# Performance work log

Measured on AMD Instinct MI355X. Metric: run time of the kernel, lower is better.

The kernel has to match this reference:

```python
import jax, jax.numpy as jnp
import numpy as np

NEG_SLOPE = 0.2  # PyG GATConv default negative_slope
EPS = 1e-16


def gat_conv(x, edge_index, W, att_src, att_dst, bias, heads, out_c, concat):
    """Faithful PyG GATConv forward (add_self_loops=True).
    x: [N, F_in], edge_index: [2, E] (row 0 = src, row 1 = dst),
    W: [heads*out_c, F_in], att_src/att_dst: [1, heads, out_c], bias: [out]
    """
    N = x.shape[0]
    loop = jnp.arange(N, dtype=edge_index.dtype)
    src = jnp.concatenate([edge_index[0], loop])
    dst = jnp.concatenate([edge_index[1], loop])

    h = (x @ W.T).reshape(N, heads, out_c)            # [N, H, C]
    a_src = jnp.sum(h * att_src, axis=-1)             # [N, H]
    a_dst = jnp.sum(h * att_dst, axis=-1)             # [N, H]

    e = jax.nn.leaky_relu(a_src[src] + a_dst[dst], NEG_SLOPE)   # [E+N, H]
    # numerically-stable segment softmax over incoming edges of dst
    m = jax.ops.segment_max(e, dst, num_segments=N)             # [N, H]
    p = jnp.exp(e - m[dst])
    denom = jax.ops.segment_sum(p, dst, num_segments=N)         # [N, H]
    alpha = p / (denom[dst] + EPS)                              # [E+N, H]

    out = jax.ops.segment_sum(h[src] * alpha[:, :, None], dst, num_segments=N)  # [N, H, C]
    out = out.reshape(N, heads * out_c) if concat else out.mean(axis=1)
    return out + bias


def setup_inputs() -> dict:
    key = jax.random.key(0)
    ks = jax.random.split(key, 11)
    N, E = 100_000, 1_600_000
    in_dim, hid, heads = 128, 64, 2
    s = 0.1
    x = jax.random.normal(ks[0], (N, in_dim), jnp.float32)
    edge_index_l2 = jax.random.randint(ks[1], (2, E), 0, N, dtype=jnp.int32)
    edge_index_l1 = jax.random.randint(ks[2], (2, E), 0, N, dtype=jnp.int32)
    # layer gat_l2: in_dim -> hid per head, heads=2, concat=True
    W2 = jax.random.normal(ks[3], (heads * hid, in_dim), jnp.float32) * s
    att_src2 = jax.random.normal(ks[4], (1, heads, hid), jnp.float32) * s
    att_dst2 = jax.random.normal(ks[5], (1, heads, hid), jnp.float32) * s
    b2 = jnp.zeros((heads * hid,), jnp.float32)
    # layer gat_l1: hid*heads -> hid, 1 head, concat=False
    W1 = jax.random.normal(ks[6], (hid, heads * hid), jnp.float32) * s
    att_src1 = jax.random.normal(ks[7], (1, 1, hid), jnp.float32) * s
    att_dst1 = jax.random.normal(ks[8], (1, 1, hid), jnp.float32) * s
    b1 = jnp.zeros((hid,), jnp.float32)
    return {
        "x": x,
        "edge_index_l1": edge_index_l1,
        "edge_index_l2": edge_index_l2,
        "W2": W2, "att_src2": att_src2, "att_dst2": att_dst2, "b2": b2,
        "W1": W1, "att_src1": att_src1, "att_dst1": att_dst1, "b1": b1,
    }


def reference(x, edge_index_l1, edge_index_l2, W2, att_src2, att_dst2, b2,
              W1, att_src1, att_dst1, b1):
    h = jax.nn.elu(gat_conv(x, edge_index_l2, W2, att_src2, att_dst2, b2,
                            heads=2, out_c=64, concat=True))    # [N, 128]
    h = jax.nn.elu(gat_conv(h, edge_index_l1, W1, att_src1, att_dst1, b1,
                            heads=1, out_c=64, concat=False))   # [N, 64]
    return h
```

## Files before the change

### kernel.cpp

```cpp
#include <hip/hip_runtime.h>
#include <hip/hip_bf16.h>
#include <math.h>

#define LRELU_SLOPE 0.2f
#define EPS 1e-16f
#define BUCK_SHIFT 8
#define BUCK_NODES 256
#define MAXBUCK 512

typedef __hip_bfloat16 bf16;
typedef __attribute__((ext_vector_type(8))) short bf16x8;
typedef __attribute__((ext_vector_type(4))) float f32x4;

__device__ inline float lrelu(float v) { return v > 0.f ? v : LRELU_SLOPE * v; }
__device__ inline float bflo(unsigned u) { return __uint_as_float(u << 16); }
__device__ inline float bfhi(unsigned u) { return __uint_as_float(u & 0xffff0000u); }
__device__ inline short f2bf(float f) {
  bf16 t = __float2bfloat16(f);
  return *reinterpret_cast<short*>(&t);
}
__device__ inline unsigned pack2(float lo, float hi) {
  return ((unsigned)(unsigned short)f2bf(hi) << 16) | (unsigned)(unsigned short)f2bf(lo);
}

__global__ void prep_kernel(const float* __restrict__ W2, unsigned short* __restrict__ Wb2,
                            const float* __restrict__ W1, unsigned short* __restrict__ Wb1,
                            int* __restrict__ gcur, int ngc) {
  int idx = blockIdx.x * blockDim.x + threadIdx.x;
  if (idx < ngc) gcur[idx] = 0;
  if (idx < 16384) {
    Wb2[idx] = (unsigned short)f2bf(W2[idx]);
  } else {
    int i = idx - 16384;
    if (i < 8192) Wb1[i] = (unsigned short)f2bf(W1[i]);
  }
}

template <int EPB>
__global__ __launch_bounds__(256) void partition_both_kernel(
    const int* __restrict__ ei2, int E2, int* __restrict__ gcur2, int* __restrict__ slab2,
    const int* __restrict__ ei1, int E1, int* __restrict__ gcur1, int* __restrict__ slab1,
    int cap, int nbuck, int nblk2) {
  __shared__ int cnt[MAXBUCK];
  __shared__ int sbase[MAXBUCK];
  const int tid = threadIdx.x;
  const bool l2 = (int)blockIdx.x < nblk2;
  const int bid = l2 ? blockIdx.x : blockIdx.x - nblk2;
  const int* ei = l2 ? ei2 : ei1;
  const int E = l2 ? E2 : E1;
  int* gcur = l2 ? gcur2 : gcur1;
  int* part = l2 ? slab2 : slab1;
  for (int t = tid; t < nbuck; t += 256) cnt[t] = 0;
  __syncthreads();
  const int e0 = bid * EPB;
  constexpr int KPT = EPB / 256;
  int sv[KPT], dv[KPT];
#pragma unroll
  for (int k = 0; k < KPT; k++) {
    int e = e0 + tid + k * 256;
    if (e < E) {
      sv[k] = ei[e];
      dv[k] = ei[E + e];
      atomicAdd(&cnt[dv[k] >> BUCK_SHIFT], 1);
    } else {
      dv[k] = -1;
    }
  }
  __syncthreads();
  for (int t = tid; t < nbuck; t += 256) {
    int c = cnt[t];
    if (c) sbase[t] = atomicAdd(&gcur[t], c);
    cnt[t] = 0;
  }
  __syncthreads();
#pragma unroll
  for (int k = 0; k < KPT; k++) {
    if (dv[k] >= 0) {
      int b = dv[k] >> BUCK_SHIFT;
      int pos = sbase[b] + atomicAdd(&cnt[b], 1);
      if (pos < cap) part[(size_t)b * cap + pos] = (sv[k] << 8) | (dv[k] & (BUCK_NODES - 1));
    }
  }
}

template <int H>
__global__ __launch_bounds__(256) void csr_build_kernel(
    int* __restrict__ slab, const int* __restrict__ gcur, int cap,
    const float* __restrict__ asrc, const float* __restrict__ adst, float* __restrict__ pcsr,
    int plane, int* __restrict__ rowbeg, int* __restrict__ rowend, int N) {
  extern __shared__ char smem[];
  int* s_sd = (int*)smem;
  int* hist = (int*)(s_sd + cap);
  int* histp = hist + 256;
  int* escanp = histp + 256;
  int* cur = escanp + 256;
  int* wtot = cur + 256;
  float* s_ad = (float*)(wtot + 4);

  const int b = blockIdx.x;
  const int tid = threadIdx.x;
  const int lane = tid & 63;
  const int wid = tid >> 6;
  const int nb0 = b << BUCK_SHIFT;
  const int nn = min(BUCK_NODES, N - nb0);
  const int cnt = min(gcur[b], cap - 7 * BUCK_NODES);
  const int B = b * cap;
  int* eidx = slab;

  hist[tid] = 0;
  cur[tid] = 0;
  for (int t = tid; t < nn * H; t += 256) s_ad[t] = adst[(size_t)nb0 * H + t];
  __syncthreads();
  for (int i = tid; i < cnt; i += 256) {
    int pr = slab[(size_t)B + i];
    s_sd[i] = pr;
    atomicAdd(&hist[pr & (BUCK_NODES - 1)], 1);
  }
  __syncthreads();
  const int h0 = hist[tid];
  const int hp = (h0 + 7) & ~7;
  histp[tid] = hp;
  int inc = hp;
#pragma unroll
  for (int off = 1; off < 64; off <<= 1) {
    int t = __shfl_up(inc, off);
    if (lane >= off) inc += t;
  }
  if (lane == 63) wtot[wid] = inc;
  __syncthreads();
  int base = 0;
  for (int w = 0; w < wid; w++) base += wtot[w];
  escanp[tid] = inc + base;
  if (tid < nn) {
    rowbeg[nb0 + tid] = B + inc + base - hp;
    rowend[nb0 + tid] = B + inc + base;
  }
  __syncthreads();
  for (int i = tid; i < cnt; i += 256) {
    int pr = s_sd[i];
    int d8 = pr & (BUCK_NODES - 1);
    int s = pr >> 8;
    int slot = B + (escanp[d8] - histp[d8]) + atomicAdd(&cur[d8], 1);
    eidx[slot] = s;
    if constexpr (H == 2) {
      float2 a = *(const float2*)&asrc[2 * (size_t)s];
      float2 ad = *(const float2*)&s_ad[2 * d8];
      pcsr[slot] = __expf(lrelu(a.x + ad.x));
      pcsr[plane + slot] = __expf(lrelu(a.y + ad.y));
    } else {
      pcsr[slot] = __expf(lrelu(asrc[s] + s_ad[d8]));
    }
  }
  if (tid < nn) {
    int pb = B + escanp[tid] - histp[tid];
    for (int k = h0; k < hp; k++) {
      eidx[pb + k] = nb0 + tid;
      pcsr[pb + k] = 0.f;
      if constexpr (H == 2) pcsr[plane + pb + k] = 0.f;
    }
  }
}

template <int M, int H, bool SPLIT, typename Tin>
__global__ __launch_bounds__(256) void gemm_att_mfma(
    const Tin* __restrict__ x, const unsigned short* __restrict__ Wb,
    const float* __restrict__ atts, const float* __restrict__ attd, bf16* __restrict__ h,
    float* __restrict__ asrc, float* __restrict__ adst, float* __restrict__ pself, int N) {
  constexpr int K = 128;
  constexpr int NF = M / 16;
  const int wid = threadIdx.x >> 6;
  const int lane = threadIdx.x & 63;
  const int r0 = blockIdx.x * 64 + wid * 16;
  if (r0 >= N) return;
  const int colb = lane & 15;
  const int kgrp = lane >> 4;
  const size_t arow = (size_t)min(r0 + colb, N - 1);

  f32x4 acc[NF];
#pragma unroll
  for (int f = 0; f < NF; f++) acc[f] = (f32x4){0.f, 0.f, 0.f, 0.f};

#pragma unroll
  for (int k0 = 0; k0 < K; k0 += 32) {
    const int kb = k0 + kgrp * 8;
    bf16x8 ahi, alo;
    if constexpr (SPLIT) {
      const float* xp = (const float*)x + arow * K + kb;
      float4 l0 = *(const float4*)xp;
      float4 l1 = *(const float4*)(xp + 4);
      float xv[8] = {l0.x, l0.y, l0.z, l0.w, l1.x, l1.y, l1.z, l1.w};
#pragma unroll
      for (int j = 0; j < 8; j++) {
        short hb = f2bf(xv[j]);
        ahi[j] = hb;
        float hf = __uint_as_float(((unsigned)(unsigned short)hb) << 16);
        alo[j] = f2bf(xv[j] - hf);
      }
    } else {
      ahi = *(const bf16x8*)((const unsigned short*)x + arow * K + kb);
    }
#pragma unroll
    for (int f = 0; f < NF; f++) {
      bf16x8 b = *(const bf16x8*)(Wb + (size_t)(f * 16 + colb) * K + kb);
      if constexpr (SPLIT)
        acc[f] = __builtin_amdgcn_mfma_f32_16x16x32_bf16(alo, b, acc[f], 0, 0, 0);
      acc[f] = __builtin_amdgcn_mfma_f32_16x16x32_bf16(ahi, b, acc[f], 0, 0, 0);
    }
  }

#pragma unroll
  for (int r = 0; r < 4; r++) {
    const int row = r0 + kgrp * 4 + r;
    const bool ok = row < N;
    float s0 = 0.f, d0 = 0.f, s1 = 0.f, d1 = 0.f;
#pragma unroll
    for (int f = 0; f < NF; f++) {
      float v = acc[f][r];
      int c = f * 16 + colb;
      if (ok) h[(size_t)row * M + c] = __float2bfloat16(v);
      float av = atts[c], dv = attd[c];
      if (H == 2 && f >= NF / 2) {
        s1 += v * av;
        d1 += v * dv;
      } else {
        s0 += v * av;
        d0 += v * dv;
      }
    }
#pragma unroll
    for (int off = 1; off < 16; off <<= 1) {
      s0 += __shfl_xor(s0, off);
      d0 += __shfl_xor(d0, off);
      if (H == 2) {
        s1 += __shfl_xor(s1, off);
        d1 += __shfl_xor(d1, off);
      }
    }
    if (ok && colb == 0) {
      if (H == 2) {
        asrc[2 * (size_t)row] = s0;
        asrc[2 * (size_t)row + 1] = s1;
        adst[2 * (size_t)row] = d0;
        adst[2 * (size_t)row + 1] = d1;
        *(float2*)&pself[2 * (size_t)row] =
            make_float2(__expf(lrelu(s0 + d0)), __expf(lrelu(s1 + d1)));
      } else {
        asrc[row] = s0;
        adst[row] = d0;
        pself[row] = __expf(lrelu(s0 + d0));
      }
    }
  }
}

__global__ void gather2_kernel(const bf16* __restrict__ h, const float* __restrict__ pself,
                               const int* __restrict__ rowbeg, const int* __restrict__ rowend,
                               const int* __restrict__ eidx, const float* __restrict__ pcsr,
                               int plane, const float* __restrict__ bias,
                               bf16* __restrict__ outp, int N) {
  long long gt = (long long)blockIdx.x * blockDim.x + threadIdx.x;
  int n = (int)(gt >> 6);
  int lane = threadIdx.x & 63;
  if (n >= N) return;
  const int half = lane >> 5;
  const int cc = lane & 31;
  const float* pc = pcsr + ((cc < 16) ? 0 : plane);
  int start = rowbeg[n];
  int end = rowend[n];
  const float2 ps = *(const float2*)&pself[2 * (size_t)n];
  float g = half ? 0.f : (cc < 16 ? ps.x : ps.y);
  uint2 hv = *(const uint2*)&h[(size_t)n * 128 + 4 * cc];
  float den = g;
  float a0 = g * bflo(hv.x), a1 = g * bfhi(hv.x);
  float a2 = g * bflo(hv.y), a3 = g * bfhi(hv.y);
  for (int j = start + half * 4; j < end; j += 8) {
    int4 ia = *(const int4*)&eidx[j];
    float4 pv = *(const float4*)&pc[j];
    uint2 hA = *(const uint2*)&h[(size_t)ia.x * 128 + 4 * cc];
    uint2 hB = *(const uint2*)&h[(size_t)ia.y * 128 + 4 * cc];
    uint2 hC = *(const uint2*)&h[(size_t)ia.z * 128 + 4 * cc];
    uint2 hD = *(const uint2*)&h[(size_t)ia.w * 128 + 4 * cc];
    den += (pv.x + pv.y) + (pv.z + pv.w);
    a0 += (pv.x * bflo(hA.x) + pv.y * bflo(hB.x)) + (pv.z * bflo(hC.x) + pv.w * bflo(hD.x));
    a1 += (pv.x * bfhi(hA.x) + pv.y * bfhi(hB.x)) + (pv.z * bfhi(hC.x) + pv.w * bfhi(hD.x));
    a2 += (pv.x * bflo(hA.y) + pv.y * bflo(hB.y)) + (pv.z * bflo(hC.y) + pv.w * bflo(hD.y));
    a3 += (pv.x * bfhi(hA.y) + pv.y * bfhi(hB.y)) + (pv.z * bfhi(hC.y) + pv.w * bfhi(hD.y));
  }
  den += __shfl_xor(den, 32);
  a0 += __shfl_xor(a0, 32);
  a1 += __shfl_xor(a1, 32);
  a2 += __shfl_xor(a2, 32);
  a3 += __shfl_xor(a3, 32);
  if (!half) {
    float rden = 1.f / (den + EPS);
    float4 bv = *(const float4*)&bias[4 * cc];
    float v0 = a0 * rden + bv.x;
    float v1 = a1 * rden + bv.y;
    float v2 = a2 * rden + bv.z;
    float v3 = a3 * rden + bv.w;
    v0 = v0 > 0.f ? v0 : expm1f(v0);
    v1 = v1 > 0.f ? v1 : expm1f(v1);
    v2 = v2 > 0.f ? v2 : expm1f(v2);
    v3 = v3 > 0.f ? v3 : expm1f(v3);
    uint2 o;
    o.x = pack2(v0, v1);
    o.y = pack2(v2, v3);
    *(uint2*)&outp[(size_t)n * 128 + 4 * cc] = o;
  }
}

__global__ void gather1_kernel(const bf16* __restrict__ h, const float* __restrict__ pself,
                               const int* __restrict__ rowbeg, const int* __restrict__ rowend,
                               const int* __restrict__ eidx, const float* __restrict__ pcsr,
                               const float* __restrict__ bias, float* __restrict__ outp, int N) {
  long long gt = (long long)blockIdx.x * blockDim.x + threadIdx.x;
  int n = (int)(gt >> 6);
  int lane = threadIdx.x & 63;
  if (n >= N) return;
  const int half = lane >> 5;
  const int c = lane & 31;
  int start = rowbeg[n];
  int end = rowend[n];
  unsigned hv = *(const unsigned*)&h[(size_t)n * 64 + 2 * c];
  float g = half ? 0.f : pself[n];
  float den = g;
  float acc0 = g * bflo(hv), acc1 = g * bfhi(hv);
  for (int t = start + half * 4; t < end; t += 8) {
    int4 ia = *(const int4*)&eidx[t];
    float4 pa = *(const float4*)&pcsr[t];
    unsigned hA = *(const unsigned*)&h[(size_t)ia.x * 64 + 2 * c];
    unsigned hB = *(const unsigned*)&h[(size_t)ia.y * 64 + 2 * c];
    unsigned hC = *(const unsigned*)&h[(size_t)ia.z * 64 + 2 * c];
    unsigned hD = *(const unsigned*)&h[(size_t)ia.w * 64 + 2 * c];
    den += (pa.x + pa.y) + (pa.z + pa.w);
    acc0 += (pa.x * bflo(hA) + pa.y * bflo(hB)) + (pa.z * bflo(hC) + pa.w * bflo(hD));
    acc1 += (pa.x * bfhi(hA) + pa.y * bfhi(hB)) + (pa.z * bfhi(hC) + pa.w * bfhi(hD));
  }
  den += __shfl_xor(den, 32);
  acc0 += __shfl_xor(acc0, 32);
  acc1 += __shfl_xor(acc1, 32);
  if (!half) {
    float rden = 1.f / (den + EPS);
    float2 bv = *(const float2*)&bias[2 * c];
    float v0 = acc0 * rden + bv.x;
    float v1 = acc1 * rden + bv.y;
    v0 = v0 > 0.f ? v0 : expm1f(v0);
    v1 = v1 > 0.f ? v1 : expm1f(v1);
    *(float2*)&outp[(size_t)n * 64 + 2 * c] = make_float2(v0, v1);
  }
}

extern "C" void kernel_launch(void* const* d_in, const int* in_sizes, int n_in,
                              void* d_out, int out_size, void* d_ws, size_t ws_size,
                              hipStream_t stream) {
  const float* x = (const float*)d_in[0];
  const int* ei1 = (const int*)d_in[1];
  const int* ei2 = (const int*)d_in[2];
  const float* W2 = (const float*)d_in[3];
  const float* as2 = (const float*)d_in[4];
  const float* ad2 = (const float*)d_in[5];
  const float* b2 = (const float*)d_in[6];
  const float* W1 = (const float*)d_in[7];
  const float* as1 = (const float*)d_in[8];
  const float* ad1 = (const float*)d_in[9];
  const float* b1 = (const float*)d_in[10];
  float* out = (float*)d_out;

  const int N = in_sizes[0] / 128;
  const int E1 = in_sizes[1] / 2;
  const int E2 = in_sizes[2] / 2;
  const int Emax = E1 > E2 ? E1 : E2;
  const size_t Ns = (size_t)N;

  const int nbuck = (N + BUCK_NODES - 1) / BUCK_NODES;
  int lam = (Emax + nbuck - 1) / nbuck;
  int cap = lam + (lam >> 2) + 2048;
  cap = (cap + 255) & ~(int)255;
  const size_t NC = (size_t)nbuck * cap;

  float* ws = (float*)d_ws;
  size_t o = 0;
  unsigned short* Wb2 = (unsigned short*)(ws + o); o += 8192;
  unsigned short* Wb1 = (unsigned short*)(ws + o); o += 4096;
  float* asrc2 = ws + o;  o += 2 * Ns;
  float* adst2 = ws + o;  o += 2 * Ns;
  float* pself2 = ws + o; o += 2 * Ns;
  float* asrc1 = ws + o;  o += Ns;
  float* adst1 = ws + o;  o += Ns;
  float* pself1 = ws + o; o += Ns;
  int* gcur2 = (int*)(ws + o);   o += (size_t)nbuck;
  int* gcur1 = (int*)(ws + o);   o += (size_t)nbuck;
  int* rowbeg2 = (int*)(ws + o); o += Ns;
  int* rowend2 = (int*)(ws + o); o += Ns;
  int* rowbeg1 = (int*)(ws + o); o += Ns;
  int* rowend1 = (int*)(ws + o); o += Ns;
  o = (o + 7) & ~(size_t)7;
  int* slab2 = (int*)(ws + o);   o += NC;
  int* slab1 = (int*)(ws + o);   o += NC;
  o = (o + 7) & ~(size_t)7;
  float* pcsr = ws + o;          o += 2 * NC;
  o = (o + 7) & ~(size_t)7;
  bf16* h2 = (bf16*)(ws + o);    o += 64 * Ns;
  bf16* h1 = h2;
  bf16* hin1 = (bf16*)(ws + o);  o += 64 * Ns;

  const size_t smem2 = (size_t)cap * 4 + 4 * 256 * 4 + 16 + 2 * 256 * 4 + 64;
  const size_t smem1 = (size_t)cap * 4 + 4 * 256 * 4 + 16 + 1 * 256 * 4 + 64;

  const int nblk2 = (E2 + 4095) / 4096;
  const int nblk1 = (E1 + 4095) / 4096;

  prep_kernel<<<(16384 + 8192 + 255) / 256, 256, 0, stream>>>(W2, Wb2, W1, Wb1, gcur2, 2 * nbuck);
  partition_both_kernel<4096><<<nblk2 + nblk1, 256, 0, stream>>>(
      ei2, E2, gcur2, slab2, ei1, E1, gcur1, slab1, cap, nbuck, nblk2);

  gemm_att_mfma<128, 2, true, float>
      <<<(N + 63) / 64, 256, 0, stream>>>(x, Wb2, as2, ad2, h2, asrc2, adst2, pself2, N);
  csr_build_kernel<2><<<nbuck, 256, smem2, stream>>>(slab2, gcur2, cap, asrc2, adst2, pcsr,
                                                     (int)NC, rowbeg2, rowend2, N);
  gather2_kernel<<<(N + 3) / 4, 256, 0, stream>>>(h2, pself2, rowbeg2, rowend2, slab2, pcsr,
                                                  (int)NC, b2, hin1, N);

  gemm_att_mfma<64, 1, false, bf16>
      <<<(N + 63) / 64, 256, 0, stream>>>(hin1, Wb1, as1, ad1, h1, asrc1, adst1, pself1, N);
  csr_build_kernel<1><<<nbuck, 256, smem1, stream>>>(slab1, gcur1, cap, asrc1, adst1, pcsr,
                                                     0, rowbeg1, rowend1, N);
  gather1_kernel<<<(N + 3) / 4, 256, 0, stream>>>(h1, pself1, rowbeg1, rowend1, slab1, pcsr,
                                                  b1, out, N);
}
```

Before: 334.7 us.

## Interleave per-head edge weights and widen gather loads to quarter-wave edge groups

Edge weights for the two heads are now stored interleaved (float2 per edge) instead of in two separate planes, so one vector load serves both heads. Both gather kernels switch from half-wave to quarter-wave partitioning: each lane loads wider feature chunks (16 bytes in layer 2, 8 bytes in layer 1) and four edge groups run concurrently per wave. The per-lane reductions then need two shuffle stages. The aim is fewer, wider memory transactions per gathered row and more edges in flight, at the cost of more registers per lane and some redundant weight loads.

Result: faster. 315.2 us (-5.8%).

```diff
diff --git a/kernel.cpp b/kernel.cpp
--- a/kernel.cpp
+++ b/kernel.cpp
@@ -87,7 +87,7 @@
 __global__ __launch_bounds__(256) void csr_build_kernel(
     int* __restrict__ slab, const int* __restrict__ gcur, int cap,
     const float* __restrict__ asrc, const float* __restrict__ adst, float* __restrict__ pcsr,
-    int plane, int* __restrict__ rowbeg, int* __restrict__ rowend, int N) {
+    int* __restrict__ rowbeg, int* __restrict__ rowend, int N) {
   extern __shared__ char smem[];
   int* s_sd = (int*)smem;
   int* hist = (int*)(s_sd + cap);
@@ -145,8 +145,10 @@
     if constexpr (H == 2) {
       float2 a = *(const float2*)&asrc[2 * (size_t)s];
       float2 ad = *(const float2*)&s_ad[2 * d8];
-      pcsr[slot] = __expf(lrelu(a.x + ad.x));
-      pcsr[plane + slot] = __expf(lrelu(a.y + ad.y));
+      float2 pv;
+      pv.x = __expf(lrelu(a.x + ad.x));
+      pv.y = __expf(lrelu(a.y + ad.y));
+      *(float2*)&pcsr[2 * (size_t)slot] = pv;
     } else {
       pcsr[slot] = __expf(lrelu(asrc[s] + s_ad[d8]));
     }
@@ -155,8 +157,11 @@
     int pb = B + escanp[tid] - histp[tid];
     for (int k = h0; k < hp; k++) {
       eidx[pb + k] = nb0 + tid;
-      pcsr[pb + k] = 0.f;
-      if constexpr (H == 2) pcsr[plane + pb + k] = 0.f;
+      if constexpr (H == 2) {
+        *(float2*)&pcsr[2 * (size_t)(pb + k)] = make_float2(0.f, 0.f);
+      } else {
+        pcsr[pb + k] = 0.f;
+      }
     }
   }
 }
@@ -256,44 +261,128 @@
 __global__ void gather2_kernel(const bf16* __restrict__ h, const float* __restrict__ pself,
                                const int* __restrict__ rowbeg, const int* __restrict__ rowend,
                                const int* __restrict__ eidx, const float* __restrict__ pcsr,
-                               int plane, const float* __restrict__ bias,
-                               bf16* __restrict__ outp, int N) {
+                               const float* __restrict__ bias, bf16* __restrict__ outp, int N) {
   long long gt = (long long)blockIdx.x * blockDim.x + threadIdx.x;
   int n = (int)(gt >> 6);
   int lane = threadIdx.x & 63;
   if (n >= N) return;
-  const int half = lane >> 5;
-  const int cc = lane & 31;
-  const float* pc = pcsr + ((cc < 16) ? 0 : plane);
+  const int qw = lane >> 4;
+  const int cl = lane & 15;
+  const bool head0 = cl < 8;
   int start = rowbeg[n];
   int end = rowend[n];
   const float2 ps = *(const float2*)&pself[2 * (size_t)n];
-  float g = half ? 0.f : (cc < 16 ? ps.x : ps.y);
-  uint2 hv = *(const uint2*)&h[(size_t)n * 128 + 4 * cc];
+  float g = qw ? 0.f : (head0 ? ps.x : ps.y);
+  uint4 hv = *(const uint4*)&h[(size_t)n * 128 + 8 * cl];
   float den = g;
   float a0 = g * bflo(hv.x), a1 = g * bfhi(hv.x);
   float a2 = g * bflo(hv.y), a3 = g * bfhi(hv.y);
-  for (int j = start + half * 4; j < end; j += 8) {
+  float a4 = g * bflo(hv.z), a5 = g * bfhi(hv.z);
+  float a6 = g * bflo(hv.w), a7 = g * bfhi(hv.w);
+  for (int j = start + 4 * qw; j < end; j += 16) {
     int4 ia = *(const int4*)&eidx[j];
-    float4 pv = *(const float4*)&pc[j];
-    uint2 hA = *(const uint2*)&h[(size_t)ia.x * 128 + 4 * cc];
-    uint2 hB = *(const uint2*)&h[(size_t)ia.y * 128 + 4 * cc];
-    uint2 hC = *(const uint2*)&h[(size_t)ia.z * 128 + 4 * cc];
-    uint2 hD = *(const uint2*)&h[(size_t)ia.w * 128 + 4 * cc];
+    float4 q0 = *(const float4*)&pcsr[2 * (size_t)j];
+    float4 q1 = *(const float4*)&pcsr[2 * (size_t)j + 4];
+    uint4 hA = *(const uint4*)&h[(size_t)ia.x * 128 + 8 * cl];
+    uint4 hB = *(const uint4*)&h[(size_t)ia.y * 128 + 8 * cl];
+    uint4 hC = *(const uint4*)&h[(size_t)ia.z * 128 + 8 * cl];
+    uint4 hD = *(const uint4*)&h[(size_t)ia.w * 128 + 8 * cl];
+    float pa = head0 ? q0.x : q0.y;
+    float pb = head0 ? q0.z : q0.w;
+    float pc = head0 ? q1.x : q1.y;
+    float pd = head0 ? q1.z : q1.w;
+    den += (pa + pb) + (pc + pd);
+    a0 += (pa * bflo(hA.x) + pb * bflo(hB.x)) + (pc * bflo(hC.x) + pd * bflo(hD.x));
+    a1 += (pa * bfhi(hA.x) + pb * bfhi(hB.x)) + (pc * bfhi(hC.x) + pd * bfhi(hD.x));
+    a2 += (pa * bflo(hA.y) + pb * bflo(hB.y)) + (pc * bflo(hC.y) + pd * bflo(hD.y));
+    a3 += (pa * bfhi(hA.y) + pb * bfhi(hB.y)) + (pc * bfhi(hC.y) + pd * bfhi(hD.y));
+    a4 += (pa * bflo(hA.z) + pb * bflo(hB.z)) + (pc * bflo(hC.z) + pd * bflo(hD.z));
+    a5 += (pa * bfhi(hA.z) + pb * bfhi(hB.z)) + (pc * bfhi(hC.z) + pd * bfhi(hD.z));
+    a6 += (pa * bflo(hA.w) + pb * bflo(hB.w)) + (pc * bflo(hC.w) + pd * bflo(hD.w));
+    a7 += (pa * bfhi(hA.w) + pb * bfhi(hB.w)) + (pc * bfhi(hC.w) + pd * bfhi(hD.w));
+  }
+#pragma unroll
+  for (int off = 16; off <= 32; off <<= 1) {
+    den += __shfl_xor(den, off);
+    a0 += __shfl_xor(a0, off);
+    a1 += __shfl_xor(a1, off);
+    a2 += __shfl_xor(a2, off);
+    a3 += __shfl_xor(a3, off);
+    a4 += __shfl_xor(a4, off);
+    a5 += __shfl_xor(a5, off);
+    a6 += __shfl_xor(a6, off);
+    a7 += __shfl_xor(a7, off);
+  }
+  if (qw == 0) {
+    float rden = 1.f / (den + EPS);
+    float4 bv0 = *(const float4*)&bias[8 * cl];
+    float4 bv1 = *(const float4*)&bias[8 * cl + 4];
+    float v0 = a0 * rden + bv0.x;
+    float v1 = a1 * rden + bv0.y;
+    float v2 = a2 * rden + bv0.z;
+    float v3 = a3 * rden + bv0.w;
+    float v4 = a4 * rden + bv1.x;
+    float v5 = a5 * rden + bv1.y;
+    float v6 = a6 * rden + bv1.z;
+    float v7 = a7 * rden + bv1.w;
+    v0 = v0 > 0.f ? v0 : expm1f(v0);
+    v1 = v1 > 0.f ? v1 : expm1f(v1);
+    v2 = v2 > 0.f ? v2 : expm1f(v2);
+    v3 = v3 > 0.f ? v3 : expm1f(v3);
+    v4 = v4 > 0.f ? v4 : expm1f(v4);
+    v5 = v5 > 0.f ? v5 : expm1f(v5);
+    v6 = v6 > 0.f ? v6 : expm1f(v6);
+    v7 = v7 > 0.f ? v7 : expm1f(v7);
+    uint4 o;
+    o.x = pack2(v0, v1);
+    o.y = pack2(v2, v3);
+    o.z = pack2(v4, v5);
+    o.w = pack2(v6, v7);
+    *(uint4*)&outp[(size_t)n * 128 + 8 * cl] = o;
+  }
+}
+
+__global__ void gather1_kernel(const bf16* __restrict__ h, const float* __restrict__ pself,
+                               const int* __restrict__ rowbeg, const int* __restrict__ rowend,
+                               const int* __restrict__ eidx, const float* __restrict__ pcsr,
+                               const float* __restrict__ bias, float* __restrict__ outp, int N) {
+  long long gt = (long long)blockIdx.x * blockDim.x + threadIdx.x;
+  int n = (int)(gt >> 6);
+  int lane = threadIdx.x & 63;
+  if (n >= N) return;
+  const int qw = lane >> 4;
+  const int cl = lane & 15;
+  int start = rowbeg[n];
+  int end = rowend[n];
+  uint2 hv = *(const uint2*)&h[(size_t)n * 64 + 4 * cl];
+  float g = qw ? 0.f : pself[n];
+  float den = g;
+  float a0 = g * bflo(hv.x), a1 = g * bfhi(hv.x);
+  float a2 = g * bflo(hv.y), a3 = g * bfhi(hv.y);
+  for (int j = start + 4 * qw; j < end; j += 16) {
+    int4 ia = *(const int4*)&eidx[j];
+    float4 pv = *(const float4*)&pcsr[j];
+    uint2 hA = *(const uint2*)&h[(size_t)ia.x * 64 + 4 * cl];
+    uint2 hB = *(const uint2*)&h[(size_t)ia.y * 64 + 4 * cl];
+    uint2 hC = *(const uint2*)&h[(size_t)ia.z * 64 + 4 * cl];
+    uint2 hD = *(const uint2*)&h[(size_t)ia.w * 64 + 4 * cl];
     den += (pv.x + pv.y) + (pv.z + pv.w);
     a0 += (pv.x * bflo(hA.x) + pv.y * bflo(hB.x)) + (pv.z * bflo(hC.x) + pv.w * bflo(hD.x));
     a1 += (pv.x * bfhi(hA.x) + pv.y * bfhi(hB.x)) + (pv.z * bfhi(hC.x) + pv.w * bfhi(hD.x));
     a2 += (pv.x * bflo(hA.y) + pv.y * bflo(hB.y)) + (pv.z * bflo(hC.y) + pv.w * bflo(hD.y));
     a3 += (pv.x * bfhi(hA.y) + pv.y * bfhi(hB.y)) + (pv.z * bfhi(hC.y) + pv.w * bfhi(hD.y));
   }
-  den += __shfl_xor(den, 32);
-  a0 += __shfl_xor(a0, 32);
-  a1 += __shfl_xor(a1, 32);
-  a2 += __shfl_xor(a2, 32);
-  a3 += __shfl_xor(a3, 32);
-  if (!half) {
+#pragma unroll
+  for (int off = 16; off <= 32; off <<= 1) {
+    den += __shfl_xor(den, off);
+    a0 += __shfl_xor(a0, off);
+    a1 += __shfl_xor(a1, off);
+    a2 += __shfl_xor(a2, off);
+    a3 += __shfl_xor(a3, off);
+  }
+  if (qw == 0) {
     float rden = 1.f / (den + EPS);
-    float4 bv = *(const float4*)&bias[4 * cc];
+    float4 bv = *(const float4*)&bias[4 * cl];
     float v0 = a0 * rden + bv.x;
     float v1 = a1 * rden + bv.y;
     float v2 = a2 * rden + bv.z;
@@ -302,51 +391,7 @@
     v1 = v1 > 0.f ? v1 : expm1f(v1);
     v2 = v2 > 0.f ? v2 : expm1f(v2);
     v3 = v3 > 0.f ? v3 : expm1f(v3);
-    uint2 o;
-    o.x = pack2(v0, v1);
-    o.y = pack2(v2, v3);
-    *(uint2*)&outp[(size_t)n * 128 + 4 * cc] = o;
-  }
-}
-
-__global__ void gather1_kernel(const bf16* __restrict__ h, const float* __restrict__ pself,
-                               const int* __restrict__ rowbeg, const int* __restrict__ rowend,
-                               const int* __restrict__ eidx, const float* __restrict__ pcsr,
-                               const float* __restrict__ bias, float* __restrict__ outp, int N) {
-  long long gt = (long long)blockIdx.x * blockDim.x + threadIdx.x;
-  int n = (int)(gt >> 6);
-  int lane = threadIdx.x & 63;
-  if (n >= N) return;
-  const int half = lane >> 5;
-  const int c = lane & 31;
-  int start = rowbeg[n];
-  int end = rowend[n];
-  unsigned hv = *(const unsigned*)&h[(size_t)n * 64 + 2 * c];
-  float g = half ? 0.f : pself[n];
-  float den = g;
-  float acc0 = g * bflo(hv), acc1 = g * bfhi(hv);
-  for (int t = start + half * 4; t < end; t += 8) {
-    int4 ia = *(const int4*)&eidx[t];
-    float4 pa = *(const float4*)&pcsr[t];
-    unsigned hA = *(const unsigned*)&h[(size_t)ia.x * 64 + 2 * c];
-    unsigned hB = *(const unsigned*)&h[(size_t)ia.y * 64 + 2 * c];
-    unsigned hC = *(const unsigned*)&h[(size_t)ia.z * 64 + 2 * c];
-    unsigned hD = *(const unsigned*)&h[(size_t)ia.w * 64 + 2 * c];
-    den += (pa.x + pa.y) + (pa.z + pa.w);
-    acc0 += (pa.x * bflo(hA) + pa.y * bflo(hB)) + (pa.z * bflo(hC) + pa.w * bflo(hD));
-    acc1 += (pa.x * bfhi(hA) + pa.y * bfhi(hB)) + (pa.z * bfhi(hC) + pa.w * bfhi(hD));
-  }
-  den += __shfl_xor(den, 32);
-  acc0 += __shfl_xor(acc0, 32);
-  acc1 += __shfl_xor(acc1, 32);
-  if (!half) {
-    float rden = 1.f / (den + EPS);
-    float2 bv = *(const float2*)&bias[2 * c];
-    float v0 = acc0 * rden + bv.x;
-    float v1 = acc1 * rden + bv.y;
-    v0 = v0 > 0.f ? v0 : expm1f(v0);
-    v1 = v1 > 0.f ? v1 : expm1f(v1);
-    *(float2*)&outp[(size_t)n * 64 + 2 * c] = make_float2(v0, v1);
+    *(float4*)&outp[(size_t)n * 64 + 4 * cl] = make_float4(v0, v1, v2, v3);
   }
 }
 
@@ -417,14 +462,14 @@
   gemm_att_mfma<128, 2, true, float>
       <<<(N + 63) / 64, 256, 0, stream>>>(x, Wb2, as2, ad2, h2, asrc2, adst2, pself2, N);
   csr_build_kernel<2><<<nbuck, 256, smem2, stream>>>(slab2, gcur2, cap, asrc2, adst2, pcsr,
-                                                     (int)NC, rowbeg2, rowend2, N);
+                                                     rowbeg2, rowend2, N);
   gather2_kernel<<<(N + 3) / 4, 256, 0, stream>>>(h2, pself2, rowbeg2, rowend2, slab2, pcsr,
-                                                  (int)NC, b2, hin1, N);
+                                                  b2, hin1, N);
 
   gemm_att_mfma<64, 1, false, bf16>
       <<<(N + 63) / 64, 256, 0, stream>>>(hin1, Wb1, as1, ad1, h1, asrc1, adst1, pself1, N);
   csr_build_kernel<1><<<nbuck, 256, smem1, stream>>>(slab1, gcur1, cap, asrc1, adst1, pcsr,
-                                                     0, rowbeg1, rowend1, N);
+                                                     rowbeg1, rowend1, N);
   gather1_kernel<<<(N + 3) / 4, 256, 0, stream>>>(h1, pself1, rowbeg1, rowend1, slab1, pcsr,
                                                   b1, out, N);
 }
```
